# Kernel optimization log

Hardware: AMD Instinct MI355X
Metric: run time of the kernel (lower is better)

The kernel has to match this reference:

```python
import jax, jax.numpy as jnp
import numpy as np

# dims
B, L, D0, P, K = 4, 512, 640, 128, 16
C, H, NL = 32, 4, 3            # hidden channels, heads, layers
DH = C // H
RAD_IN = P + 2                 # pair feat + bppm + distance
HPT = 0.3                      # high_prob_threshold


def _build_edges(bppm, coords):
    """Backbone + kNN + high-prob edges per sample, deduped, flattened over batch."""
    src_all, dst_all = [], []
    for b in range(B):
        s_bb = np.arange(L - 1); d_bb = np.arange(1, L)
        srcs = [s_bb, d_bb]; dsts = [d_bb, s_bb]
        c = coords[b]
        d2 = ((c[:, None, :] - c[None, :, :]) ** 2).sum(-1)
        nn = np.argsort(d2, axis=1)[:, 1:K + 1]            # exclude self
        s_knn = np.repeat(np.arange(L), K); d_knn = nn.reshape(-1)
        srcs += [s_knn, d_knn]; dsts += [d_knn, s_knn]
        iu, ju = np.triu_indices(L, 2)                      # |i-j| > 1
        m = bppm[b][iu, ju] >= HPT
        hs, hd = iu[m], ju[m]
        srcs += [hs, hd]; dsts += [hd, hs]
        e = np.unique(np.stack([np.concatenate(srcs), np.concatenate(dsts)], 1), axis=0)
        src_all.append(e[:, 0] + b * L); dst_all.append(e[:, 1] + b * L)
    return np.concatenate(src_all).astype(np.int32), np.concatenate(dst_all).astype(np.int32)


def setup_inputs() -> dict:
    rng = np.random.default_rng(0)
    sequence_rep = rng.standard_normal((B, L, D0)).astype(np.float32)
    pair_rep = rng.standard_normal((B, L, L, P)).astype(np.float32)
    u = rng.random((B, L, L)).astype(np.float32)
    bppm = (0.5 * (u + u.transpose(0, 2, 1))) ** 8          # sparse-ish symmetric BPPM
    initial_coords = (10.0 * rng.standard_normal((B, L, 3))).astype(np.float32)
    edge_src, edge_dst = _build_edges(bppm, initial_coords)

    def w(*shape):
        fan = shape[-2] if len(shape) >= 2 else shape[-1]
        return (rng.standard_normal(shape) / np.sqrt(fan)).astype(np.float32)

    inp = dict(
        sequence_rep=jnp.asarray(sequence_rep), pair_rep=jnp.asarray(pair_rep),
        bppm=jnp.asarray(bppm.astype(np.float32)), initial_coords=jnp.asarray(initial_coords),
        edge_src=jnp.asarray(edge_src), edge_dst=jnp.asarray(edge_dst),
        Win0=jnp.asarray(w(D0, C)), Win1=jnp.asarray(w(1, C)),
        Wr1=jnp.asarray(w(NL, RAD_IN, 64)), br1=jnp.zeros((NL, 64), jnp.float32),
        Wr2=jnp.asarray(w(NL, 64, 4 * C)), br2=jnp.zeros((NL, 4 * C), jnp.float32),
        Wm00=jnp.asarray(w(NL, C, C)), Wm01=jnp.asarray(w(NL, C, C)),
        Wm10=jnp.asarray(w(NL, C, C)), Wm11=jnp.asarray(w(NL, C, C)),
        Wq=jnp.asarray(w(NL, C, C)), Wself0=jnp.asarray(w(NL, C, C)), Wself1=jnp.asarray(w(NL, C, C)),
        gamma0=jnp.ones((NL, C), jnp.float32), beta0=jnp.zeros((NL, C), jnp.float32),
        gamma1=jnp.ones((NL, C), jnp.float32), Wout=jnp.asarray(w(C, 1)),
    )
    return inp


def _forward(sequence_rep, pair_rep, bppm, initial_coords,
             Win0, Win1, Wr1, br1, Wr2, br2, Wm00, Wm01, Wm10, Wm11,
             Wq, Wself0, Wself1, gamma0, beta0, gamma1, Wout, edge_src, edge_dst):
    N = B * L
    x = initial_coords.reshape(N, 3)
    h0 = sequence_rep.reshape(N, D0) @ Win0                  # [N,C] degree-0
    h1 = x[:, None, :] * Win1[0][None, :, None]              # [N,C,3] degree-1
    src, dst = edge_src, edge_dst
    rel = x[dst] - x[src]
    r = jnp.sqrt(jnp.sum(rel * rel, -1) + 1e-12)             # [E]
    rhat = rel / (r[:, None] + 1e-8)                         # Y1 spherical harmonic dir
    b_idx, si, di = src // L, src % L, dst % L
    ef = jnp.concatenate([pair_rep[b_idx, si, di], bppm[b_idx, si, di][:, None], r[:, None]], -1)

    for l in range(NL):
        rad = jax.nn.relu(ef @ Wr1[l] + br1[l]) @ Wr2[l] + br2[l]   # [E,4C] radial weights
        w00, w01, w10, w11 = jnp.split(rad, 4, axis=-1)
        h0s, h1s = h0[src], h1[src]
        dot1 = jnp.einsum('ecd,ed->ec', h1s, rhat)                  # deg1 -> deg0 path
        m0 = w00 * (h0s @ Wm00[l]) + w01 * (dot1 @ Wm01[l])          # [E,C]
        m1 = (w11[:, :, None] * jnp.einsum('ecd,cf->efd', h1s, Wm11[l])
              + (w10 * (h0s @ Wm10[l]))[:, :, None] * rhat[:, None, :])  # [E,C,3]
        # multi-head attention over incoming edges
        q = (h0 @ Wq[l]).reshape(N, H, DH)
        k = m0.reshape(-1, H, DH)
        logit = jnp.sum(q[dst] * k, -1) / np.sqrt(DH)                # [E,H]
        mx = jax.ops.segment_max(logit, dst, num_segments=N)
        mx = jnp.where(jnp.isfinite(mx), mx, 0.0)
        a = jnp.exp(logit - mx[dst])
        den = jax.ops.segment_sum(a, dst, num_segments=N)
        alpha = a / (den[dst] + 1e-9)                                # [E,H]
        agg0 = jax.ops.segment_sum(alpha[:, :, None] * k, dst, num_segments=N).reshape(N, C)
        agg1 = jax.ops.segment_sum(alpha[:, :, None, None] * m1.reshape(-1, H, DH, 3),
                                   dst, num_segments=N).reshape(N, C, 3)
        h0 = h0 + agg0 @ Wself0[l]
        h1 = h1 + jnp.einsum('ncd,cf->nfd', agg1, Wself1[l])
        # norms: LayerNorm on deg-0, equivariant norm-gating on deg-1
        mu = h0.mean(-1, keepdims=True)
        h0 = (h0 - mu) / jnp.sqrt(h0.var(-1, keepdims=True) + 1e-5) * gamma0[l] + beta0[l]
        nrm = jnp.sqrt(jnp.sum(h1 * h1, -1) + 1e-12)                 # [N,C]
        nln = (nrm - nrm.mean(-1, keepdims=True)) / jnp.sqrt(nrm.var(-1, keepdims=True) + 1e-5) * gamma1[l]
        h1 = h1 * (nln / (nrm + 1e-8))[:, :, None]
    delta = jnp.einsum('ncd,co->nod', h1, Wout)[:, 0, :]             # fiber_out {'1':1}
    return (x + delta).reshape(B, L, 3)


def reference(sequence_rep, pair_rep, bppm, initial_coords, edge_src, edge_dst,
              Win0, Win1, Wr1, br1, Wr2, br2, Wm00, Wm01, Wm10, Wm11,
              Wq, Wself0, Wself1, gamma0, beta0, gamma1, Wout):
    return _forward(sequence_rep, pair_rep, bppm, initial_coords,
                    Win0, Win1, Wr1, br1, Wr2, br2, Wm00, Wm01, Wm10, Wm11,
                    Wq, Wself0, Wself1, gamma0, beta0, gamma1, Wout, edge_src, edge_dst)
```

## Files before the change

### kernel.cpp

```cpp
#include <hip/hip_runtime.h>
#include <hip/hip_bf16.h>
#include <hip/hip_fp16.h>
#include <math.h>

#define BB 4
#define LL 512
#define D0 640
#define PP 128
#define CC 32
#define NLAYER 3
#define NN (BB*LL)
#define RADIN 130

typedef __attribute__((ext_vector_type(8))) short bf16x8;
typedef __attribute__((ext_vector_type(4))) float f32x4;

__device__ __forceinline__ short f2b(float v) {
    __hip_bfloat16 h = __float2bfloat16(v);
    short s; __builtin_memcpy(&s, &h, 2); return s;
}
__device__ __forceinline__ unsigned short f2h(float v) {
    __half h = __float2half(v);
    unsigned short s; __builtin_memcpy(&s, &h, 2); return s;
}
__device__ __forceinline__ float h2f(unsigned short s) {
    __half h; __builtin_memcpy(&h, &s, 2); return __half2float(h);
}


__global__ __launch_bounds__(64) void k_init_h0(const float* __restrict__ seq,
                                                const float* __restrict__ Win0,
                                                float* __restrict__ h0) {
    const int n = blockIdx.x, lane = threadIdx.x;
    const int c = lane & 31, half = lane >> 5;
    const float* s = seq + (size_t)n * D0;
    float acc = 0.f;
    const int i0 = half * (D0 / 2), i1 = i0 + (D0 / 2);
    for (int i = i0; i < i1; ++i) acc = fmaf(s[i], Win0[i * CC + c], acc);
    acc += __shfl_xor(acc, 32);
    if (lane < 32) h0[n * CC + c] = acc;
}

__global__ void k_init_h1(const float* __restrict__ x, const float* __restrict__ Win1,
                          float* __restrict__ h1, int* __restrict__ deg) {
    int idx = blockIdx.x * blockDim.x + threadIdx.x;
    if (idx < NN) deg[idx] = 0;
    if (idx >= NN * CC) return;
    int n = idx >> 5, c = idx & 31;
    float w = Win1[c];
    const float* xp = x + n * 3;
    float* hp = h1 + (size_t)n * 96 + c * 3;
    hp[0] = xp[0] * w; hp[1] = xp[1] * w; hp[2] = xp[2] * w;
}

__global__ __launch_bounds__(256) void k_edge_setup(
    const int* __restrict__ src, const int* __restrict__ dst,
    const float* __restrict__ x,
    const float* __restrict__ pair, const float* __restrict__ bppm,
    float* __restrict__ rhat, int* __restrict__ deg,
    short* __restrict__ efb, int E)
{
    int e = blockIdx.x * 4 + (threadIdx.x >> 6);
    int lane = threadIdx.x & 63;
    if (e >= E) return;
    int s = src[e], d = dst[e];
    float dx = x[d * 3 + 0] - x[s * 3 + 0];
    float dy = x[d * 3 + 1] - x[s * 3 + 1];
    float dz = x[d * 3 + 2] - x[s * 3 + 2];
    float r = sqrtf(dx * dx + dy * dy + dz * dz + 1e-12f);
    float ir = 1.f / (r + 1e-8f);
    int b = s / LL, si = s % LL, di = d % LL;
    size_t prow = ((size_t)b * LL + si) * LL + di;
    const float* pr = pair + prow * PP;
    short* out = efb + (size_t)e * 160;
    out[lane] = f2b(pr[lane]);
    out[64 + lane] = f2b(pr[64 + lane]);
    if (lane < 32) {
        float v = 0.f;
        if (lane == 0) v = bppm[prow];
        else if (lane == 1) v = r;
        out[128 + lane] = f2b(v);
    }
    if (lane < 3) rhat[e * 3 + lane] = (lane == 0 ? dx : lane == 1 ? dy : dz) * ir;
    if (lane == 0) atomicAdd(&deg[d], 1);
}

__global__ __launch_bounds__(64) void k_scan(const int* __restrict__ deg,
                                             int* __restrict__ rowptr,
                                             int* __restrict__ cursor) {
    const int lane = threadIdx.x;
    const int base = lane * 32;
    int loc[32]; int s = 0;
    for (int i = 0; i < 32; ++i) { loc[i] = deg[base + i]; s += loc[i]; }
    int pre = s;
    for (int off = 1; off < 64; off <<= 1) {
        int t = __shfl_up(pre, off);
        if (lane >= off) pre += t;
    }
    pre -= s;
    int run = pre;
    for (int i = 0; i < 32; ++i) { rowptr[base + i] = run; cursor[base + i] = 0; run += loc[i]; }
    if (lane == 63) rowptr[NN] = run;
}

__global__ void k_scatter(const int* __restrict__ dst, const int* __restrict__ rowptr,
                          int* __restrict__ cursor, int* __restrict__ eperm, int E) {
    int e = blockIdx.x * blockDim.x + threadIdx.x;
    if (e >= E) return;
    int d = dst[e];
    int pos = atomicAdd(&cursor[d], 1);
    eperm[e] = rowptr[d] + pos;
}

__global__ void k_pack(const float* __restrict__ Wr1, const float* __restrict__ Wr2,
                       short* __restrict__ W1p, short* __restrict__ W2p) {
    int t = blockIdx.x * blockDim.x + threadIdx.x;
    const int tot1 = NLAYER * 5 * 4 * 64 * 8;
    const int tot2 = NLAYER * 2 * 8 * 64 * 8;
    if (t < tot1) {
        int j = t & 7; int r = t >> 3;
        int ln = r & 63; r >>= 6;
        int cb = r & 3; r >>= 2;
        int kb = r % 5; int l = r / 5;
        int row = kb * 32 + (ln >> 4) * 8 + j;
        int col = cb * 16 + (ln & 15);
        float v = (row < RADIN) ? Wr1[((size_t)l * RADIN + row) * 64 + col] : 0.f;
        W1p[t] = f2b(v);
    } else if (t < tot1 + tot2) {
        int t2 = t - tot1;
        int j = t2 & 7; int r = t2 >> 3;
        int ln = r & 63; r >>= 6;
        int cb = r & 7; r >>= 3;
        int kb = r & 1; int l = r >> 1;
        int row = kb * 32 + (ln >> 4) * 8 + j;
        int col = cb * 16 + (ln & 15);
        W2p[t2] = f2b(Wr2[((size_t)l * 64 + row) * 128 + col]);
    }
}

__global__ __launch_bounds__(256) void k_nodepre(
    int l, const float* __restrict__ h0, const float* __restrict__ h1,
    const float* __restrict__ Wq, const float* __restrict__ Wm00,
    const float* __restrict__ Wm10, const float* __restrict__ Wm11,
    float* __restrict__ qbuf, float* __restrict__ P00,
    float* __restrict__ P10, float* __restrict__ P11)
{
    __shared__ float sh0[8][32], sh1[8][96];
    const int c = threadIdx.x & 31, hw = threadIdx.x >> 5;
    const int n = blockIdx.x * 8 + hw;
    sh0[hw][c] = h0[n * CC + c];
    const float* hp = h1 + (size_t)n * 96 + c * 3;
    sh1[hw][c * 3 + 0] = hp[0]; sh1[hw][c * 3 + 1] = hp[1]; sh1[hw][c * 3 + 2] = hp[2];
    const float* WqL  = Wq   + l * 1024;
    const float* W00L = Wm00 + l * 1024;
    const float* W10L = Wm10 + l * 1024;
    const float* W11L = Wm11 + l * 1024;
    float q = 0.f, p00 = 0.f, p10 = 0.f, px = 0.f, py = 0.f, pz = 0.f;
    for (int i = 0; i < 32; ++i) {
        float a = sh0[hw][i];
        q   = fmaf(a, WqL[i * 32 + c], q);
        p00 = fmaf(a, W00L[i * 32 + c], p00);
        p10 = fmaf(a, W10L[i * 32 + c], p10);
        float w = W11L[i * 32 + c];
        px = fmaf(sh1[hw][i * 3 + 0], w, px);
        py = fmaf(sh1[hw][i * 3 + 1], w, py);
        pz = fmaf(sh1[hw][i * 3 + 2], w, pz);
    }
    qbuf[n * 32 + c] = q; P00[n * 32 + c] = p00; P10[n * 32 + c] = p10;
    float* pp = P11 + (size_t)n * 96 + c * 3;
    pp[0] = px; pp[1] = py; pp[2] = pz;
}

__global__ __launch_bounds__(256) void k_radedge(
    int l, int E,
    const int* __restrict__ src,
    const float* __restrict__ rhat,
    const short* __restrict__ efb,
    const short* __restrict__ W1p,
    const short* __restrict__ W2p,
    const float* __restrict__ br1,
    const float* __restrict__ br2,
    const float* __restrict__ Wm01,
    const float* __restrict__ h1,
    const float* __restrict__ P00,
    const float* __restrict__ P10,
    const float* __restrict__ P11,
    const int* __restrict__ eperm,
    unsigned short* __restrict__ mbuf)
{
    __shared__ short s_hid[4][16][72];
    __shared__ float s_rad[64][132];
    __shared__ float sW[1024];
    const int lane = threadIdx.x & 63, wv = threadIdx.x >> 6;
    const int r16 = lane & 15, q4 = lane >> 4;
    const int eb = blockIdx.x * 64;
    const int e0 = eb + wv * 16;

    for (int i = threadIdx.x; i < 1024; i += 256) sW[i] = Wm01[l * 1024 + i];

    f32x4 acc0 = {0.f,0.f,0.f,0.f}, acc1 = {0.f,0.f,0.f,0.f};
    f32x4 acc2 = {0.f,0.f,0.f,0.f}, acc3 = {0.f,0.f,0.f,0.f};
    int row = e0 + r16; if (row >= E) row = E - 1;
    const short* arow = efb + (size_t)row * 160 + q4 * 8;
    const short* b1b = W1p + (size_t)l * (5 * 4 * 64 * 8) + lane * 8;
    for (int kb = 0; kb < 5; ++kb) {
        bf16x8 af = *(const bf16x8*)(arow + kb * 32);
        const short* bp = b1b + kb * (4 * 64 * 8);
        bf16x8 b0 = *(const bf16x8*)(bp);
        bf16x8 b1v = *(const bf16x8*)(bp + 64 * 8);
        bf16x8 b2v = *(const bf16x8*)(bp + 2 * 64 * 8);
        bf16x8 b3v = *(const bf16x8*)(bp + 3 * 64 * 8);
        acc0 = __builtin_amdgcn_mfma_f32_16x16x32_bf16(af, b0,  acc0, 0, 0, 0);
        acc1 = __builtin_amdgcn_mfma_f32_16x16x32_bf16(af, b1v, acc1, 0, 0, 0);
        acc2 = __builtin_amdgcn_mfma_f32_16x16x32_bf16(af, b2v, acc2, 0, 0, 0);
        acc3 = __builtin_amdgcn_mfma_f32_16x16x32_bf16(af, b3v, acc3, 0, 0, 0);
    }
    {
        f32x4 a[4] = {acc0, acc1, acc2, acc3};
        for (int cb = 0; cb < 4; ++cb) {
            int col = cb * 16 + r16;
            float b = br1[l * 64 + col];
            for (int i = 0; i < 4; ++i) {
                float v = fmaxf(a[cb][i] + b, 0.f);
                s_hid[wv][q4 * 4 + i][col] = f2b(v);
            }
        }
    }
    f32x4 o[8];
    for (int cb = 0; cb < 8; ++cb) { o[cb].x=0.f; o[cb].y=0.f; o[cb].z=0.f; o[cb].w=0.f; }
    const short* b2b = W2p + (size_t)l * (2 * 8 * 64 * 8) + lane * 8;
    for (int kb = 0; kb < 2; ++kb) {
        bf16x8 af = *(const bf16x8*)(&s_hid[wv][r16][kb * 32 + q4 * 8]);
        const short* bp = b2b + kb * (8 * 64 * 8);
        for (int cb = 0; cb < 8; ++cb) {
            bf16x8 bf = *(const bf16x8*)(bp + cb * (64 * 8));
            o[cb] = __builtin_amdgcn_mfma_f32_16x16x32_bf16(af, bf, o[cb], 0, 0, 0);
        }
    }
    for (int cb = 0; cb < 8; ++cb) {
        int col = cb * 16 + r16;
        float b = br2[l * 128 + col];
        for (int i = 0; i < 4; ++i) {
            s_rad[wv * 16 + q4 * 4 + i][col] = o[cb][i] + b;
        }
    }
    __syncthreads();

    const int hw = threadIdx.x >> 5;
    const int c = lane & 31;
    const int base = lane & 32;
    for (int it = 0; it < 8; ++it) {
        const int el = hw * 8 + it;
        const int e = eb + el;
        if (e >= E) break;
        const int s = src[e];
        const float r0 = rhat[e * 3 + 0], r1 = rhat[e * 3 + 1], r2 = rhat[e * 3 + 2];
        const float* hp = h1 + (size_t)s * 96 + c * 3;
        const float dot = hp[0] * r0 + hp[1] * r1 + hp[2] * r2;
        float t1 = 0.f;
        for (int i = 0; i < 32; ++i) {
            float di = __shfl(dot, base + i);
            t1 = fmaf(di, sW[i * 32 + c], t1);
        }
        const float w00 = s_rad[el][c],      w01 = s_rad[el][32 + c];
        const float w10 = s_rad[el][64 + c], w11 = s_rad[el][96 + c];
        const float m0 = fmaf(w00, P00[s * 32 + c], w01 * t1);
        const float u10 = w10 * P10[s * 32 + c];
        const float* pp = P11 + (size_t)s * 96 + c * 3;
        unsigned short* mp = mbuf + (size_t)eperm[e] * 128;
        mp[c] = f2h(m0);
        mp[32 + c * 3 + 0] = f2h(fmaf(w11, pp[0], u10 * r0));
        mp[32 + c * 3 + 1] = f2h(fmaf(w11, pp[1], u10 * r1));
        mp[32 + c * 3 + 2] = f2h(fmaf(w11, pp[2], u10 * r2));
    }
}

__global__ __launch_bounds__(256) void k_node(
    int l, const int* __restrict__ rowptr,
    const unsigned short* __restrict__ mbuf,
    const float* __restrict__ qbuf_in,
    float* __restrict__ h0, float* __restrict__ h1,
    const float* __restrict__ Ws0, const float* __restrict__ Ws1,
    const float* __restrict__ gam0, const float* __restrict__ bet0,
    const float* __restrict__ gam1,
    const float* __restrict__ Wq, const float* __restrict__ Wm00,
    const float* __restrict__ Wm10, const float* __restrict__ Wm11,
    float* __restrict__ qout, float* __restrict__ P00,
    float* __restrict__ P10, float* __restrict__ P11,
    const float* __restrict__ x, const float* __restrict__ Wout,
    float* __restrict__ outp)
{
    const int n = blockIdx.x;
    const int tid = threadIdx.x;
    const int hw = tid >> 5;
    const int c = tid & 31;
    __shared__ float s_part[8][32][6];
    __shared__ float s_a0[32], s_a1[96];
    __shared__ float s_hn[128];

    const float qc = qbuf_in[n * 32 + c];
    const int st = rowptr[n], en = rowptr[n + 1];

    float m_run = -INFINITY, l_run = 0.f;
    float a0 = 0.f, a1x = 0.f, a1y = 0.f, a1z = 0.f;
    for (int idx = st + hw; idx < en; idx += 8) {
        const unsigned short* row = mbuf + (size_t)idx * 128;
        const float kc = h2f(row[c]);
        const float mv0 = h2f(row[32 + c * 3 + 0]);
        const float mv1 = h2f(row[32 + c * 3 + 1]);
        const float mv2 = h2f(row[32 + c * 3 + 2]);
        float p = qc * kc;
        p += __shfl_xor(p, 1); p += __shfl_xor(p, 2); p += __shfl_xor(p, 4);
        const float logit = p * 0.35355339059327373f;
        const float mn = fmaxf(m_run, logit);
        const float sc = __expf(m_run - mn);
        const float w  = __expf(logit - mn);
        l_run = fmaf(l_run, sc, w);
        a0  = fmaf(a0,  sc, w * kc);
        a1x = fmaf(a1x, sc, w * mv0);
        a1y = fmaf(a1y, sc, w * mv1);
        a1z = fmaf(a1z, sc, w * mv2);
        m_run = mn;
    }
    s_part[hw][c][0] = m_run; s_part[hw][c][1] = l_run;
    s_part[hw][c][2] = a0;
    s_part[hw][c][3] = a1x; s_part[hw][c][4] = a1y; s_part[hw][c][5] = a1z;
    __syncthreads();

    if (tid < 32) {
        float M = s_part[0][c][0], L = s_part[0][c][1], A0 = s_part[0][c][2];
        float Ax = s_part[0][c][3], Ay = s_part[0][c][4], Az = s_part[0][c][5];
        for (int k = 1; k < 8; ++k) {
            const float m2 = s_part[k][c][0];
            if (m2 == -INFINITY) continue;
            const float mn = fmaxf(M, m2);
            const float sa = (M == -INFINITY) ? 0.f : __expf(M - mn);
            const float sb = __expf(m2 - mn);
            L  = L  * sa + s_part[k][c][1] * sb;
            A0 = A0 * sa + s_part[k][c][2] * sb;
            Ax = Ax * sa + s_part[k][c][3] * sb;
            Ay = Ay * sa + s_part[k][c][4] * sb;
            Az = Az * sa + s_part[k][c][5] * sb;
            M = mn;
        }
        const float inv = 1.0f / (L + 1e-9f);
        s_a0[c] = A0 * inv;
        s_a1[c * 3 + 0] = Ax * inv;
        s_a1[c * 3 + 1] = Ay * inv;
        s_a1[c * 3 + 2] = Az * inv;
    }
    __syncthreads();

    if (tid < 32) {
        float x0 = h0[n * CC + c];
        {
            const float* W = Ws0 + l * 1024;
            for (int i = 0; i < 32; ++i) x0 = fmaf(s_a0[i], W[i * 32 + c], x0);
        }
        float mu = x0;
        mu += __shfl_xor(mu, 1); mu += __shfl_xor(mu, 2); mu += __shfl_xor(mu, 4);
        mu += __shfl_xor(mu, 8); mu += __shfl_xor(mu, 16);
        mu *= (1.f / 32.f);
        float sq = x0 * x0;
        sq += __shfl_xor(sq, 1); sq += __shfl_xor(sq, 2); sq += __shfl_xor(sq, 4);
        sq += __shfl_xor(sq, 8); sq += __shfl_xor(sq, 16);
        float var = sq * (1.f / 32.f) - mu * mu;
        float h0n = (x0 - mu) * rsqrtf(var + 1e-5f) * gam0[l * 32 + c] + bet0[l * 32 + c];
        s_hn[c] = h0n;
        if (l + 1 < NLAYER) h0[n * CC + c] = h0n;

        const float* hp = h1 + (size_t)n * 96 + c * 3;
        float v0 = hp[0], v1 = hp[1], v2 = hp[2];
        {
            const float* W = Ws1 + l * 1024;
            for (int i = 0; i < 32; ++i) {
                float w = W[i * 32 + c];
                v0 = fmaf(s_a1[i * 3 + 0], w, v0);
                v1 = fmaf(s_a1[i * 3 + 1], w, v1);
                v2 = fmaf(s_a1[i * 3 + 2], w, v2);
            }
        }
        float nrm = sqrtf(v0 * v0 + v1 * v1 + v2 * v2 + 1e-12f);
        float mu2 = nrm;
        mu2 += __shfl_xor(mu2, 1); mu2 += __shfl_xor(mu2, 2); mu2 += __shfl_xor(mu2, 4);
        mu2 += __shfl_xor(mu2, 8); mu2 += __shfl_xor(mu2, 16);
        mu2 *= (1.f / 32.f);
        float sq2 = nrm * nrm;
        sq2 += __shfl_xor(sq2, 1); sq2 += __shfl_xor(sq2, 2); sq2 += __shfl_xor(sq2, 4);
        sq2 += __shfl_xor(sq2, 8); sq2 += __shfl_xor(sq2, 16);
        float var2 = sq2 * (1.f / 32.f) - mu2 * mu2;
        float nln = (nrm - mu2) * rsqrtf(var2 + 1e-5f) * gam1[l * 32 + c];
        float scl = nln / (nrm + 1e-8f);
        float w0 = v0 * scl, w1 = v1 * scl, w2 = v2 * scl;
        s_hn[32 + c * 3 + 0] = w0;
        s_hn[32 + c * 3 + 1] = w1;
        s_hn[32 + c * 3 + 2] = w2;
        if (l + 1 < NLAYER) {
            float* hq = h1 + (size_t)n * 96 + c * 3;
            hq[0] = w0; hq[1] = w1; hq[2] = w2;
        } else {
            const float wo = Wout[c];
            float d0 = w0 * wo, d1 = w1 * wo, d2 = w2 * wo;
            d0 += __shfl_xor(d0, 1); d1 += __shfl_xor(d1, 1); d2 += __shfl_xor(d2, 1);
            d0 += __shfl_xor(d0, 2); d1 += __shfl_xor(d1, 2); d2 += __shfl_xor(d2, 2);
            d0 += __shfl_xor(d0, 4); d1 += __shfl_xor(d1, 4); d2 += __shfl_xor(d2, 4);
            d0 += __shfl_xor(d0, 8); d1 += __shfl_xor(d1, 8); d2 += __shfl_xor(d2, 8);
            d0 += __shfl_xor(d0, 16); d1 += __shfl_xor(d1, 16); d2 += __shfl_xor(d2, 16);
            if (c == 0) {
                outp[n * 3 + 0] = x[n * 3 + 0] + d0;
                outp[n * 3 + 1] = x[n * 3 + 1] + d1;
                outp[n * 3 + 2] = x[n * 3 + 2] + d2;
            }
        }
    }

    if (l + 1 < NLAYER) {
        __syncthreads();
        const int grp = tid >> 5;
        if (grp < 4) {
            const int lp = l + 1;
            if (grp == 0) {
                const float* W = Wq + lp * 1024;
                float acc = 0.f;
                for (int i = 0; i < 32; ++i) acc = fmaf(s_hn[i], W[i * 32 + c], acc);
                qout[n * 32 + c] = acc;
            } else if (grp == 1) {
                const float* W = Wm00 + lp * 1024;
                float acc = 0.f;
                for (int i = 0; i < 32; ++i) acc = fmaf(s_hn[i], W[i * 32 + c], acc);
                P00[n * 32 + c] = acc;
            } else if (grp == 2) {
                const float* W = Wm10 + lp * 1024;
                float acc = 0.f;
                for (int i = 0; i < 32; ++i) acc = fmaf(s_hn[i], W[i * 32 + c], acc);
                P10[n * 32 + c] = acc;
            } else {
                const float* W = Wm11 + lp * 1024;
                float px = 0.f, py = 0.f, pz = 0.f;
                for (int i = 0; i < 32; ++i) {
                    float w = W[i * 32 + c];
                    px = fmaf(s_hn[32 + i * 3 + 0], w, px);
                    py = fmaf(s_hn[32 + i * 3 + 1], w, py);
                    pz = fmaf(s_hn[32 + i * 3 + 2], w, pz);
                }
                float* pp = P11 + (size_t)n * 96 + c * 3;
                pp[0] = px; pp[1] = py; pp[2] = pz;
            }
        }
    }
}

extern "C" void kernel_launch(void* const* d_in, const int* in_sizes, int n_in,
                              void* d_out, int out_size, void* d_ws, size_t ws_size,
                              hipStream_t stream) {
    const float* seq  = (const float*)d_in[0];
    const float* pair = (const float*)d_in[1];
    const float* bppm = (const float*)d_in[2];
    const float* x    = (const float*)d_in[3];
    const int*   src  = (const int*)d_in[4];
    const int*   dst  = (const int*)d_in[5];
    const float* Win0 = (const float*)d_in[6];
    const float* Win1 = (const float*)d_in[7];
    const float* Wr1  = (const float*)d_in[8];
    const float* br1  = (const float*)d_in[9];
    const float* Wr2  = (const float*)d_in[10];
    const float* br2  = (const float*)d_in[11];
    const float* Wm00 = (const float*)d_in[12];
    const float* Wm01 = (const float*)d_in[13];
    const float* Wm10 = (const float*)d_in[14];
    const float* Wm11 = (const float*)d_in[15];
    const float* Wq   = (const float*)d_in[16];
    const float* Ws0  = (const float*)d_in[17];
    const float* Ws1  = (const float*)d_in[18];
    const float* gam0 = (const float*)d_in[19];
    const float* bet0 = (const float*)d_in[20];
    const float* gam1 = (const float*)d_in[21];
    const float* Wout = (const float*)d_in[22];
    const int E = in_sizes[4];

    char* w = (char*)d_ws;
    auto alloc = [&](size_t nbytes) {
        void* p = (void*)w;
        w += (nbytes + 255) & ~(size_t)255;
        return p;
    };
    float* h0    = (float*)alloc((size_t)NN * CC * 4);
    float* h1    = (float*)alloc((size_t)NN * CC * 3 * 4);
    float* rhat  = (float*)alloc((size_t)E * 3 * 4);
    unsigned short* mbuf = (unsigned short*)alloc((size_t)E * 128 * 2);
    int* deg     = (int*)alloc((size_t)NN * 4);
    int* rowptr  = (int*)alloc((size_t)(NN + 1) * 4);
    int* cursor  = (int*)alloc((size_t)NN * 4);
    int* eperm   = (int*)alloc((size_t)E * 4);
    short* efb   = (short*)alloc((size_t)E * 160 * 2);
    short* W1p   = (short*)alloc((size_t)NLAYER * 5 * 4 * 64 * 8 * 2);
    short* W2p   = (short*)alloc((size_t)NLAYER * 2 * 8 * 64 * 8 * 2);
    float* qbuf  = (float*)alloc((size_t)NN * 32 * 4);
    float* P00   = (float*)alloc((size_t)NN * 32 * 4);
    float* P10   = (float*)alloc((size_t)NN * 32 * 4);
    float* P11   = (float*)alloc((size_t)NN * 96 * 4);

    const int TB = 256;
    k_init_h0<<<NN, 64, 0, stream>>>(seq, Win0, h0);
    k_init_h1<<<(NN * CC + TB - 1) / TB, TB, 0, stream>>>(x, Win1, h1, deg);
    k_edge_setup<<<(E + 3) / 4, 256, 0, stream>>>(src, dst, x, pair, bppm,
                                                  rhat, deg, efb, E);
    k_scan<<<1, 64, 0, stream>>>(deg, rowptr, cursor);
    k_scatter<<<(E + TB - 1) / TB, TB, 0, stream>>>(dst, rowptr, cursor, eperm, E);
    {
        int tot = NLAYER * 5 * 4 * 64 * 8 + NLAYER * 2 * 8 * 64 * 8;
        k_pack<<<(tot + TB - 1) / TB, TB, 0, stream>>>(Wr1, Wr2, W1p, W2p);
    }
    k_nodepre<<<NN / 8, 256, 0, stream>>>(0, h0, h1, Wq, Wm00, Wm10, Wm11,
                                          qbuf, P00, P10, P11);

    for (int l = 0; l < NLAYER; ++l) {
        k_radedge<<<(E + 63) / 64, 256, 0, stream>>>(l, E, src, rhat, efb, W1p, W2p,
                                                     br1, br2, Wm01, h1,
                                                     P00, P10, P11, eperm, mbuf);
        k_node<<<NN, 256, 0, stream>>>(l, rowptr, mbuf, qbuf, h0, h1,
                                       Ws0, Ws1, gam0, bet0, gam1,
                                       Wq, Wm00, Wm10, Wm11,
                                       qbuf, P00, P10, P11,
                                       x, Wout, (float*)d_out);
    }
}
```

Baseline: 834.6 us.

## Precompute per-node Wm01 projection of h1 and fuse init kernels

Uses linearity to move the Wm01 projection of h1 out of the per-edge loop in the radial/edge kernel and into per-node precompute (k_nodepre and the tail of k_node), stored as a new P01 buffer. Each edge then needs only a 3-element dot with rhat instead of 32 shuffles and FMAs plus loading Wm01 into shared memory. Radial weights are kept in shared memory as fp16 instead of fp32, which shrinks the LDS footprint. The three setup kernels (init_h0, init_h1, pack) are merged into one launch. In exchange it adds an extra node buffer and more gather traffic per edge (96 floats), and the fp16 radial weights lose some precision.

```diff
diff --git a/kernel.cpp b/kernel.cpp
--- a/kernel.cpp
+++ b/kernel.cpp
@@ -27,30 +27,56 @@
     __half h; __builtin_memcpy(&h, &s, 2); return __half2float(h);
 }
 
-
-__global__ __launch_bounds__(64) void k_init_h0(const float* __restrict__ seq,
-                                                const float* __restrict__ Win0,
-                                                float* __restrict__ h0) {
-    const int n = blockIdx.x, lane = threadIdx.x;
-    const int c = lane & 31, half = lane >> 5;
-    const float* s = seq + (size_t)n * D0;
-    float acc = 0.f;
-    const int i0 = half * (D0 / 2), i1 = i0 + (D0 / 2);
-    for (int i = i0; i < i1; ++i) acc = fmaf(s[i], Win0[i * CC + c], acc);
-    acc += __shfl_xor(acc, 32);
-    if (lane < 32) h0[n * CC + c] = acc;
-}
-
-__global__ void k_init_h1(const float* __restrict__ x, const float* __restrict__ Win1,
-                          float* __restrict__ h1, int* __restrict__ deg) {
-    int idx = blockIdx.x * blockDim.x + threadIdx.x;
-    if (idx < NN) deg[idx] = 0;
-    if (idx >= NN * CC) return;
-    int n = idx >> 5, c = idx & 31;
-    float w = Win1[c];
-    const float* xp = x + n * 3;
-    float* hp = h1 + (size_t)n * 96 + c * 3;
-    hp[0] = xp[0] * w; hp[1] = xp[1] * w; hp[2] = xp[2] * w;
+__global__ __launch_bounds__(256) void k_init(
+    const float* __restrict__ seq, const float* __restrict__ Win0,
+    const float* __restrict__ x, const float* __restrict__ Win1,
+    const float* __restrict__ Wr1, const float* __restrict__ Wr2,
+    float* __restrict__ h0, float* __restrict__ h1, int* __restrict__ deg,
+    short* __restrict__ W1p, short* __restrict__ W2p)
+{
+    const int b = blockIdx.x;
+    if (b < 512) {
+        const int n = b * 4 + (threadIdx.x >> 6);
+        const int lane = threadIdx.x & 63;
+        const int c = lane & 31, half = lane >> 5;
+        const float* s = seq + (size_t)n * D0;
+        float acc = 0.f;
+        const int i0 = half * (D0 / 2), i1 = i0 + (D0 / 2);
+        for (int i = i0; i < i1; ++i) acc = fmaf(s[i], Win0[i * CC + c], acc);
+        acc += __shfl_xor(acc, 32);
+        if (lane < 32) h0[n * CC + c] = acc;
+    } else if (b < 768) {
+        const int idx = (b - 512) * 256 + threadIdx.x;
+        if (idx < NN) deg[idx] = 0;
+        const int n = idx >> 5, c = idx & 31;
+        const float w = Win1[c];
+        const float* xp = x + n * 3;
+        float* hp = h1 + (size_t)n * 96 + c * 3;
+        hp[0] = xp[0] * w; hp[1] = xp[1] * w; hp[2] = xp[2] * w;
+    } else {
+        const int t = (b - 768) * 256 + threadIdx.x;
+        const int tot1 = NLAYER * 5 * 4 * 64 * 8;
+        const int tot2 = NLAYER * 2 * 8 * 64 * 8;
+        if (t < tot1) {
+            int j = t & 7; int r = t >> 3;
+            int ln = r & 63; r >>= 6;
+            int cb = r & 3; r >>= 2;
+            int kb = r % 5; int l = r / 5;
+            int row = kb * 32 + (ln >> 4) * 8 + j;
+            int col = cb * 16 + (ln & 15);
+            float v = (row < RADIN) ? Wr1[((size_t)l * RADIN + row) * 64 + col] : 0.f;
+            W1p[t] = f2b(v);
+        } else if (t < tot1 + tot2) {
+            int t2 = t - tot1;
+            int j = t2 & 7; int r = t2 >> 3;
+            int ln = r & 63; r >>= 6;
+            int cb = r & 7; r >>= 3;
+            int kb = r & 1; int l = r >> 1;
+            int row = kb * 32 + (ln >> 4) * 8 + j;
+            int col = cb * 16 + (ln & 15);
+            W2p[t2] = f2b(Wr2[((size_t)l * 64 + row) * 128 + col]);
+        }
+    }
 }
 
 __global__ __launch_bounds__(256) void k_edge_setup(
@@ -112,38 +138,13 @@
     eperm[e] = rowptr[d] + pos;
 }
 
-__global__ void k_pack(const float* __restrict__ Wr1, const float* __restrict__ Wr2,
-                       short* __restrict__ W1p, short* __restrict__ W2p) {
-    int t = blockIdx.x * blockDim.x + threadIdx.x;
-    const int tot1 = NLAYER * 5 * 4 * 64 * 8;
-    const int tot2 = NLAYER * 2 * 8 * 64 * 8;
-    if (t < tot1) {
-        int j = t & 7; int r = t >> 3;
-        int ln = r & 63; r >>= 6;
-        int cb = r & 3; r >>= 2;
-        int kb = r % 5; int l = r / 5;
-        int row = kb * 32 + (ln >> 4) * 8 + j;
-        int col = cb * 16 + (ln & 15);
-        float v = (row < RADIN) ? Wr1[((size_t)l * RADIN + row) * 64 + col] : 0.f;
-        W1p[t] = f2b(v);
-    } else if (t < tot1 + tot2) {
-        int t2 = t - tot1;
-        int j = t2 & 7; int r = t2 >> 3;
-        int ln = r & 63; r >>= 6;
-        int cb = r & 7; r >>= 3;
-        int kb = r & 1; int l = r >> 1;
-        int row = kb * 32 + (ln >> 4) * 8 + j;
-        int col = cb * 16 + (ln & 15);
-        W2p[t2] = f2b(Wr2[((size_t)l * 64 + row) * 128 + col]);
-    }
-}
-
 __global__ __launch_bounds__(256) void k_nodepre(
     int l, const float* __restrict__ h0, const float* __restrict__ h1,
     const float* __restrict__ Wq, const float* __restrict__ Wm00,
     const float* __restrict__ Wm10, const float* __restrict__ Wm11,
+    const float* __restrict__ Wm01,
     float* __restrict__ qbuf, float* __restrict__ P00,
-    float* __restrict__ P10, float* __restrict__ P11)
+    float* __restrict__ P10, float* __restrict__ P11, float* __restrict__ P01)
 {
     __shared__ float sh0[8][32], sh1[8][96];
     const int c = threadIdx.x & 31, hw = threadIdx.x >> 5;
@@ -155,20 +156,26 @@
     const float* W00L = Wm00 + l * 1024;
     const float* W10L = Wm10 + l * 1024;
     const float* W11L = Wm11 + l * 1024;
-    float q = 0.f, p00 = 0.f, p10 = 0.f, px = 0.f, py = 0.f, pz = 0.f;
+    const float* W01L = Wm01 + l * 1024;
+    float q = 0.f, p00 = 0.f, p10 = 0.f;
+    float px = 0.f, py = 0.f, pz = 0.f;
+    float ox = 0.f, oy = 0.f, oz = 0.f;
     for (int i = 0; i < 32; ++i) {
         float a = sh0[hw][i];
         q   = fmaf(a, WqL[i * 32 + c], q);
         p00 = fmaf(a, W00L[i * 32 + c], p00);
         p10 = fmaf(a, W10L[i * 32 + c], p10);
+        float h1x = sh1[hw][i * 3 + 0], h1y = sh1[hw][i * 3 + 1], h1z = sh1[hw][i * 3 + 2];
         float w = W11L[i * 32 + c];
-        px = fmaf(sh1[hw][i * 3 + 0], w, px);
-        py = fmaf(sh1[hw][i * 3 + 1], w, py);
-        pz = fmaf(sh1[hw][i * 3 + 2], w, pz);
+        px = fmaf(h1x, w, px); py = fmaf(h1y, w, py); pz = fmaf(h1z, w, pz);
+        float w2 = W01L[i * 32 + c];
+        ox = fmaf(h1x, w2, ox); oy = fmaf(h1y, w2, oy); oz = fmaf(h1z, w2, oz);
     }
     qbuf[n * 32 + c] = q; P00[n * 32 + c] = p00; P10[n * 32 + c] = p10;
     float* pp = P11 + (size_t)n * 96 + c * 3;
     pp[0] = px; pp[1] = py; pp[2] = pz;
+    float* op = P01 + (size_t)n * 96 + c * 3;
+    op[0] = ox; op[1] = oy; op[2] = oz;
 }
 
 __global__ __launch_bounds__(256) void k_radedge(
@@ -180,23 +187,19 @@
     const short* __restrict__ W2p,
     const float* __restrict__ br1,
     const float* __restrict__ br2,
-    const float* __restrict__ Wm01,
-    const float* __restrict__ h1,
     const float* __restrict__ P00,
     const float* __restrict__ P10,
     const float* __restrict__ P11,
+    const float* __restrict__ P01,
     const int* __restrict__ eperm,
     unsigned short* __restrict__ mbuf)
 {
     __shared__ short s_hid[4][16][72];
-    __shared__ float s_rad[64][132];
-    __shared__ float sW[1024];
+    __shared__ unsigned short s_radh[64][130];
     const int lane = threadIdx.x & 63, wv = threadIdx.x >> 6;
     const int r16 = lane & 15, q4 = lane >> 4;
     const int eb = blockIdx.x * 64;
     const int e0 = eb + wv * 16;
-
-    for (int i = threadIdx.x; i < 1024; i += 256) sW[i] = Wm01[l * 1024 + i];
 
     f32x4 acc0 = {0.f,0.f,0.f,0.f}, acc1 = {0.f,0.f,0.f,0.f};
     f32x4 acc2 = {0.f,0.f,0.f,0.f}, acc3 = {0.f,0.f,0.f,0.f};
@@ -241,29 +244,23 @@
         int col = cb * 16 + r16;
         float b = br2[l * 128 + col];
         for (int i = 0; i < 4; ++i) {
-            s_rad[wv * 16 + q4 * 4 + i][col] = o[cb][i] + b;
+            s_radh[wv * 16 + q4 * 4 + i][col] = f2h(o[cb][i] + b);
         }
     }
     __syncthreads();
 
     const int hw = threadIdx.x >> 5;
     const int c = lane & 31;
-    const int base = lane & 32;
     for (int it = 0; it < 8; ++it) {
         const int el = hw * 8 + it;
         const int e = eb + el;
         if (e >= E) break;
         const int s = src[e];
         const float r0 = rhat[e * 3 + 0], r1 = rhat[e * 3 + 1], r2 = rhat[e * 3 + 2];
-        const float* hp = h1 + (size_t)s * 96 + c * 3;
-        const float dot = hp[0] * r0 + hp[1] * r1 + hp[2] * r2;
-        float t1 = 0.f;
-        for (int i = 0; i < 32; ++i) {
-            float di = __shfl(dot, base + i);
-            t1 = fmaf(di, sW[i * 32 + c], t1);
-        }
-        const float w00 = s_rad[el][c],      w01 = s_rad[el][32 + c];
-        const float w10 = s_rad[el][64 + c], w11 = s_rad[el][96 + c];
+        const float w00 = h2f(s_radh[el][c]),      w01 = h2f(s_radh[el][32 + c]);
+        const float w10 = h2f(s_radh[el][64 + c]), w11 = h2f(s_radh[el][96 + c]);
+        const float* q01 = P01 + (size_t)s * 96 + c * 3;
+        const float t1 = r0 * q01[0] + r1 * q01[1] + r2 * q01[2];
         const float m0 = fmaf(w00, P00[s * 32 + c], w01 * t1);
         const float u10 = w10 * P10[s * 32 + c];
         const float* pp = P11 + (size_t)s * 96 + c * 3;
@@ -285,8 +282,9 @@
     const float* __restrict__ gam1,
     const float* __restrict__ Wq, const float* __restrict__ Wm00,
     const float* __restrict__ Wm10, const float* __restrict__ Wm11,
+    const float* __restrict__ Wm01,
     float* __restrict__ qout, float* __restrict__ P00,
-    float* __restrict__ P10, float* __restrict__ P11,
+    float* __restrict__ P10, float* __restrict__ P11, float* __restrict__ P01,
     const float* __restrict__ x, const float* __restrict__ Wout,
     float* __restrict__ outp)
 {
@@ -417,35 +415,44 @@
     if (l + 1 < NLAYER) {
         __syncthreads();
         const int grp = tid >> 5;
-        if (grp < 4) {
-            const int lp = l + 1;
-            if (grp == 0) {
-                const float* W = Wq + lp * 1024;
-                float acc = 0.f;
-                for (int i = 0; i < 32; ++i) acc = fmaf(s_hn[i], W[i * 32 + c], acc);
-                qout[n * 32 + c] = acc;
-            } else if (grp == 1) {
-                const float* W = Wm00 + lp * 1024;
-                float acc = 0.f;
-                for (int i = 0; i < 32; ++i) acc = fmaf(s_hn[i], W[i * 32 + c], acc);
-                P00[n * 32 + c] = acc;
-            } else if (grp == 2) {
-                const float* W = Wm10 + lp * 1024;
-                float acc = 0.f;
-                for (int i = 0; i < 32; ++i) acc = fmaf(s_hn[i], W[i * 32 + c], acc);
-                P10[n * 32 + c] = acc;
-            } else {
-                const float* W = Wm11 + lp * 1024;
-                float px = 0.f, py = 0.f, pz = 0.f;
-                for (int i = 0; i < 32; ++i) {
-                    float w = W[i * 32 + c];
-                    px = fmaf(s_hn[32 + i * 3 + 0], w, px);
-                    py = fmaf(s_hn[32 + i * 3 + 1], w, py);
-                    pz = fmaf(s_hn[32 + i * 3 + 2], w, pz);
-                }
-                float* pp = P11 + (size_t)n * 96 + c * 3;
-                pp[0] = px; pp[1] = py; pp[2] = pz;
+        const int lp = l + 1;
+        if (grp == 0) {
+            const float* W = Wq + lp * 1024;
+            float acc = 0.f;
+            for (int i = 0; i < 32; ++i) acc = fmaf(s_hn[i], W[i * 32 + c], acc);
+            qout[n * 32 + c] = acc;
+        } else if (grp == 1) {
+            const float* W = Wm00 + lp * 1024;
+            float acc = 0.f;
+            for (int i = 0; i < 32; ++i) acc = fmaf(s_hn[i], W[i * 32 + c], acc);
+            P00[n * 32 + c] = acc;
+        } else if (grp == 2) {
+            const float* W = Wm10 + lp * 1024;
+            float acc = 0.f;
+            for (int i = 0; i < 32; ++i) acc = fmaf(s_hn[i], W[i * 32 + c], acc);
+            P10[n * 32 + c] = acc;
+        } else if (grp == 3) {
+            const float* W = Wm11 + lp * 1024;
+            float px = 0.f, py = 0.f, pz = 0.f;
+            for (int i = 0; i < 32; ++i) {
+                float w = W[i * 32 + c];
+                px = fmaf(s_hn[32 + i * 3 + 0], w, px);
+                py = fmaf(s_hn[32 + i * 3 + 1], w, py);
+                pz = fmaf(s_hn[32 + i * 3 + 2], w, pz);
             }
+            float* pp = P11 + (size_t)n * 96 + c * 3;
+            pp[0] = px; pp[1] = py; pp[2] = pz;
+        } else if (grp == 4) {
+            const float* W = Wm01 + lp * 1024;
+            float px = 0.f, py = 0.f, pz = 0.f;
+            for (int i = 0; i < 32; ++i) {
+                float w = W[i * 32 + c];
+                px = fmaf(s_hn[32 + i * 3 + 0], w, px);
+                py = fmaf(s_hn[32 + i * 3 + 1], w, py);
+                pz = fmaf(s_hn[32 + i * 3 + 2], w, pz);
+            }
+            float* pp = P01 + (size_t)n * 96 + c * 3;
+            pp[0] = px; pp[1] = py; pp[2] = pz;
         }
     }
 }
@@ -499,29 +506,26 @@
     float* P00   = (float*)alloc((size_t)NN * 32 * 4);
     float* P10   = (float*)alloc((size_t)NN * 32 * 4);
     float* P11   = (float*)alloc((size_t)NN * 96 * 4);
+    float* P01   = (float*)alloc((size_t)NN * 96 * 4);
 
     const int TB = 256;
-    k_init_h0<<<NN, 64, 0, stream>>>(seq, Win0, h0);
-    k_init_h1<<<(NN * CC + TB - 1) / TB, TB, 0, stream>>>(x, Win1, h1, deg);
+    k_init<<<984, 256, 0, stream>>>(seq, Win0, x, Win1, Wr1, Wr2,
+                                    h0, h1, deg, W1p, W2p);
     k_edge_setup<<<(E + 3) / 4, 256, 0, stream>>>(src, dst, x, pair, bppm,
                                                   rhat, deg, efb, E);
     k_scan<<<1, 64, 0, stream>>>(deg, rowptr, cursor);
     k_scatter<<<(E + TB - 1) / TB, TB, 0, stream>>>(dst, rowptr, cursor, eperm, E);
-    {
-        int tot = NLAYER * 5 * 4 * 64 * 8 + NLAYER * 2 * 8 * 64 * 8;
-        k_pack<<<(tot + TB - 1) / TB, TB, 0, stream>>>(Wr1, Wr2, W1p, W2p);
-    }
-    k_nodepre<<<NN / 8, 256, 0, stream>>>(0, h0, h1, Wq, Wm00, Wm10, Wm11,
-                                          qbuf, P00, P10, P11);
+    k_nodepre<<<NN / 8, 256, 0, stream>>>(0, h0, h1, Wq, Wm00, Wm10, Wm11, Wm01,
+                                          qbuf, P00, P10, P11, P01);
 
     for (int l = 0; l < NLAYER; ++l) {
         k_radedge<<<(E + 63) / 64, 256, 0, stream>>>(l, E, src, rhat, efb, W1p, W2p,
-                                                     br1, br2, Wm01, h1,
-                                                     P00, P10, P11, eperm, mbuf);
+                                                     br1, br2,
+                                                     P00, P10, P11, P01, eperm, mbuf);
         k_node<<<NN, 256, 0, stream>>>(l, rowptr, mbuf, qbuf, h0, h1,
                                        Ws0, Ws1, gam0, bet0, gam1,
-                                       Wq, Wm00, Wm10, Wm11,
-                                       qbuf, P00, P10, P11,
+                                       Wq, Wm00, Wm10, Wm11, Wm01,
+                                       qbuf, P00, P10, P11, P01,
                                        x, Wout, (float*)d_out);
     }
 }
```

After: 822.4 us. No clear change (-1.5%).
